# Kernel optimization log

Measured on AMD Instinct MI355X. Metric: run time of the kernel, lower is better.

Reference implementation:

```python
import jax, jax.numpy as jnp
import numpy as np

DIM = 1024
NUM_HEADS = 16
HEAD_DIM = DIM // NUM_HEADS  # 64
MAX_LABELS = 8
B, SQ, SKV = 2, 2048, 2048


def setup_inputs() -> dict:
    key = jax.random.key(0)
    ks = jax.random.split(key, 12)
    s = 0.02
    return {
        "visual_features": jax.random.normal(ks[0], (B, SQ, DIM), jnp.float32),
        "audio_features": jax.random.normal(ks[1], (B, SKV, DIM), jnp.float32),
        "audio_labels": jax.random.randint(ks[2], (B,), 0, MAX_LABELS),
        "Wq": jax.random.normal(ks[3], (DIM, DIM), jnp.float32) * s,
        "bq": jnp.zeros((DIM,), jnp.float32),
        "Wk": jax.random.normal(ks[4], (DIM, DIM), jnp.float32) * s,
        "bk": jnp.zeros((DIM,), jnp.float32),
        "Wv": jax.random.normal(ks[5], (DIM, DIM), jnp.float32) * s,
        "bv": jnp.zeros((DIM,), jnp.float32),
        "Wo": jax.random.normal(ks[6], (DIM, DIM), jnp.float32) * s,
        "bo": jnp.zeros((DIM,), jnp.float32),
        "label_emb": jax.random.normal(ks[7], (MAX_LABELS, HEAD_DIM), jnp.float32),
    }


def _lrope_emb(label_emb, labels, seq_len, dtype):
    # inv_freq over head_dim (buffer, recomputed)
    inv_freq = 1.0 / (10000.0 ** (jnp.arange(0, HEAD_DIM, 2, dtype=jnp.float32) / HEAD_DIM))
    pos = jnp.arange(seq_len, dtype=dtype)
    freqs = jnp.outer(pos, inv_freq)                       # [S, hd/2]
    emb = jnp.concatenate([jnp.sin(freqs), jnp.cos(freqs)], axis=-1)  # [S, hd]
    lab = label_emb[labels]                                # [B, hd]
    return emb[None, :, :] * lab[:, None, :]               # [B, S, hd]


def reference(visual_features, audio_features, audio_labels,
              Wq, bq, Wk, bk, Wv, bv, Wo, bo, label_emb):
    b, sq, _ = visual_features.shape
    skv = audio_features.shape[1]
    scale = HEAD_DIM ** -0.5

    q = visual_features @ Wq.T + bq                        # [B, Sq, D]
    k = audio_features @ Wk.T + bk                         # [B, Skv, D]
    v = audio_features @ Wv.T + bv

    q = q.reshape(b, sq, NUM_HEADS, HEAD_DIM)
    k = k.reshape(b, skv, NUM_HEADS, HEAD_DIM)
    v = v.reshape(b, skv, NUM_HEADS, HEAD_DIM)

    # L-RoPE additive embedding on K (per-head broadcast of the head_dim-sized emb)
    emb = _lrope_emb(label_emb, audio_labels, skv, k.dtype)  # [B, Skv, hd]
    k = k + emb[:, :, None, :]

    scores = jnp.einsum('bqhd,bkhd->bhqk', q, k) * scale   # [B, H, Sq, Skv]
    attn = jax.nn.softmax(scores, axis=-1)                 # dropout = identity (eval)
    out = jnp.einsum('bhqk,bkhd->bqhd', attn, v)           # [B, Sq, H, hd]
    out = out.reshape(b, sq, DIM)
    return out @ Wo.T + bo
```

## Files before the change

### kernel.cpp

```cpp
#include <hip/hip_runtime.h>
#include <hip/hip_bf16.h>


typedef short s16x8 __attribute__((ext_vector_type(8)));
typedef float f32x4 __attribute__((ext_vector_type(4)));

__device__ __forceinline__ short f2bf(float f) {
    unsigned u = __float_as_uint(f);
    u = u + 0x7fffu + ((u >> 16) & 1u);
    return (short)(u >> 16);
}

#define GLDS16(g, l)                                                          \
    __builtin_amdgcn_global_load_lds(                                         \
        (const __attribute__((address_space(1))) void*)(g),                   \
        (__attribute__((address_space(3))) void*)(l), 16, 0, 0)

__global__ __launch_bounds__(256)
void cvt_all(const float* __restrict__ vis, const float* __restrict__ aud,
             const float* __restrict__ Wq, const float* __restrict__ Wk,
             const float* __restrict__ Wv, const float* __restrict__ Wo,
             short* __restrict__ visB, short* __restrict__ audB,
             short* __restrict__ WqB, short* __restrict__ WkB,
             short* __restrict__ WvB, short* __restrict__ WoB)
{
    const int bid = blockIdx.x;
    const float* src; short* dst; int vec0;
    if (bid < 2048)      { src = vis; dst = visB; vec0 = bid * 256; }
    else if (bid < 4096) { src = aud; dst = audB; vec0 = (bid - 2048) * 256; }
    else {
        const int r = bid - 4096, w = r >> 9, lb = r & 511;
        vec0 = lb * 256;
        if      (w == 0) { src = Wq; dst = WqB; }
        else if (w == 1) { src = Wk; dst = WkB; }
        else if (w == 2) { src = Wv; dst = WvB; }
        else             { src = Wo; dst = WoB; }
    }
    const int i = (vec0 + threadIdx.x) * 8;
    float4 a = *(const float4*)(src + i);
    float4 b = *(const float4*)(src + i + 4);
    s16x8 o;
    o[0]=f2bf(a.x); o[1]=f2bf(a.y); o[2]=f2bf(a.z); o[3]=f2bf(a.w);
    o[4]=f2bf(b.x); o[5]=f2bf(b.y); o[6]=f2bf(b.z); o[7]=f2bf(b.w);
    *(s16x8*)(dst + i) = o;
}

__global__ __launch_bounds__(256)
void gemm_qkv(const short* __restrict__ visB, const short* __restrict__ audB,
              const short* __restrict__ WqB, const short* __restrict__ WkB,
              const short* __restrict__ WvB,
              const float* __restrict__ bq, const float* __restrict__ bk,
              const float* __restrict__ bv,
              short* __restrict__ outQ, short* __restrict__ outK,
              short* __restrict__ outVt,
              const int* __restrict__ labels, const float* __restrict__ lemb)
{
    __shared__ __align__(16) short As[2][128 * 64];
    __shared__ __align__(16) short Bs[2][128 * 64];
    const int tid  = threadIdx.x;
    const int lane = tid & 63;
    const int wid  = tid >> 6;
    const int z    = blockIdx.z;
    const int rowBase = blockIdx.y * 128;
    const int colBase = blockIdx.x * 128;
    const int wr = (wid >> 1) * 64;
    const int wc = (wid & 1) * 64;
    const short* X = (z == 0) ? visB : audB;
    const short* W = (z == 0) ? WqB : (z == 1) ? WkB : WvB;
    const float* bias = (z == 0) ? bq : (z == 1) ? bk : bv;

    f32x4 acc[4][4] = {};

    auto stage = [&](int buf, int k0) {
        #pragma unroll
        for (int c = 0; c < 4; ++c) {
            const int u   = (wid * 4 + c) * 64 + lane;
            const int row = u >> 3;
            const int k8a = (u & 7) ^ (row & 7);
            GLDS16(X + (size_t)(rowBase + row) * 1024 + k0 + k8a * 8,
                   &As[buf][(wid * 4 + c) * 512]);
            GLDS16(W + (size_t)(colBase + row) * 1024 + k0 + k8a * 8,
                   &Bs[buf][(wid * 4 + c) * 512]);
        }
    };

    stage(0, 0);
    __syncthreads();

    for (int t = 0; t < 16; ++t) {
        const int cur = t & 1;
        if (t < 15) stage(cur ^ 1, (t + 1) * 64);
        #pragma unroll
        for (int ks = 0; ks < 2; ++ks) {
            const int kb = ks * 64 + ((lane >> 4) << 4);
            s16x8 af[4], bfv[4];
            #pragma unroll
            for (int m = 0; m < 4; ++m) {
                const int row = wr + m * 16 + (lane & 15);
                af[m] = *(const s16x8*)((const char*)&As[cur][0] + row * 128 + (kb ^ ((row & 7) << 4)));
            }
            #pragma unroll
            for (int n = 0; n < 4; ++n) {
                const int row = wc + n * 16 + (lane & 15);
                bfv[n] = *(const s16x8*)((const char*)&Bs[cur][0] + row * 128 + (kb ^ ((row & 7) << 4)));
            }
            #pragma unroll
            for (int m = 0; m < 4; ++m)
                #pragma unroll
                for (int n = 0; n < 4; ++n)
                    acc[m][n] = __builtin_amdgcn_mfma_f32_16x16x32_bf16(af[m], bfv[n], acc[m][n], 0, 0, 0);
        }
        __syncthreads();
    }

    if (z == 2) {
        char* tb = (char*)&As[0][0] + wid * 8192;
        const int b  = rowBase >> 11;
        const int h  = (colBase + wc) >> 6;
        const int kvbase = (rowBase & 2047) + wr;
        #pragma unroll
        for (int m = 0; m < 4; ++m) {
            #pragma unroll
            for (int r = 0; r < 4; ++r) {
                const int kvl = m * 16 + ((lane >> 4) << 2) + r;
                #pragma unroll
                for (int n = 0; n < 4; ++n) {
                    const int hd = n * 16 + (lane & 15);
                    const float v = acc[m][n][r] + bias[colBase + wc + hd];
                    *(short*)(tb + hd * 128 + ((kvl * 2) ^ ((hd & 7) << 4))) = f2bf(v);
                }
            }
        }
        asm volatile("s_waitcnt lgkmcnt(0)" ::: "memory");
        #pragma unroll
        for (int c = 0; c < 8; ++c) {
            const int u  = c * 64 + lane;
            const int hd = u >> 3;
            const int kc = u & 7;
            s16x8 vv = *(const s16x8*)(tb + hd * 128 + ((kc * 16) ^ ((hd & 7) << 4)));
            *(s16x8*)(outVt + ((size_t)(b * 16 + h) * 64 + hd) * 2048 + kvbase + kc * 8) = vv;
        }
    } else {
        short* Co = (z == 0) ? outQ : outK;
        #pragma unroll
        for (int m = 0; m < 4; ++m) {
            #pragma unroll
            for (int r = 0; r < 4; ++r) {
                const int grow = rowBase + wr + m * 16 + ((lane >> 4) << 2) + r;
                #pragma unroll
                for (int n = 0; n < 4; ++n) {
                    const int gcol = colBase + wc + n * 16 + (lane & 15);
                    float v = acc[m][n][r] + bias[gcol];
                    if (z == 0) {
                        v *= 0.125f;
                    } else {
                        const int bb = grow >> 11;
                        const int ss = grow & 2047;
                        const int hd = gcol & 63;
                        const int fi = hd & 31;
                        const float ang = (float)ss * __expf((float)fi * (-9.210340371976184f / 32.0f));
                        const float tr  = (hd < 32) ? sinf(ang) : cosf(ang);
                        v += tr * lemb[labels[bb] * 64 + hd];
                    }
                    Co[(size_t)grow * 1024 + gcol] = f2bf(v);
                }
            }
        }
    }
}

__global__ __launch_bounds__(256)
void gemm_out(const short* __restrict__ X, const short* __restrict__ W,
              const float* __restrict__ bias, float* __restrict__ Cf)
{
    __shared__ __align__(16) short As[2][128 * 64];
    __shared__ __align__(16) short Bs[2][128 * 64];
    const int tid  = threadIdx.x;
    const int lane = tid & 63;
    const int wid  = tid >> 6;
    const int rowBase = blockIdx.y * 128;
    const int colBase = blockIdx.x * 128;
    const int wr = (wid >> 1) * 64;
    const int wc = (wid & 1) * 64;

    f32x4 acc[4][4] = {};

    auto stage = [&](int buf, int k0) {
        #pragma unroll
        for (int c = 0; c < 4; ++c) {
            const int u   = (wid * 4 + c) * 64 + lane;
            const int row = u >> 3;
            const int k8a = (u & 7) ^ (row & 7);
            GLDS16(X + (size_t)(rowBase + row) * 1024 + k0 + k8a * 8,
                   &As[buf][(wid * 4 + c) * 512]);
            GLDS16(W + (size_t)(colBase + row) * 1024 + k0 + k8a * 8,
                   &Bs[buf][(wid * 4 + c) * 512]);
        }
    };

    stage(0, 0);
    __syncthreads();

    for (int t = 0; t < 16; ++t) {
        const int cur = t & 1;
        if (t < 15) stage(cur ^ 1, (t + 1) * 64);
        #pragma unroll
        for (int ks = 0; ks < 2; ++ks) {
            const int kb = ks * 64 + ((lane >> 4) << 4);
            s16x8 af[4], bfv[4];
            #pragma unroll
            for (int m = 0; m < 4; ++m) {
                const int row = wr + m * 16 + (lane & 15);
                af[m] = *(const s16x8*)((const char*)&As[cur][0] + row * 128 + (kb ^ ((row & 7) << 4)));
            }
            #pragma unroll
            for (int n = 0; n < 4; ++n) {
                const int row = wc + n * 16 + (lane & 15);
                bfv[n] = *(const s16x8*)((const char*)&Bs[cur][0] + row * 128 + (kb ^ ((row & 7) << 4)));
            }
            #pragma unroll
            for (int m = 0; m < 4; ++m)
                #pragma unroll
                for (int n = 0; n < 4; ++n)
                    acc[m][n] = __builtin_amdgcn_mfma_f32_16x16x32_bf16(af[m], bfv[n], acc[m][n], 0, 0, 0);
        }
        __syncthreads();
    }

    #pragma unroll
    for (int m = 0; m < 4; ++m) {
        #pragma unroll
        for (int r = 0; r < 4; ++r) {
            const int grow = rowBase + wr + m * 16 + ((lane >> 4) << 2) + r;
            #pragma unroll
            for (int n = 0; n < 4; ++n) {
                const int gcol = colBase + wc + n * 16 + (lane & 15);
                Cf[(size_t)grow * 1024 + gcol] = acc[m][n][r] + bias[gcol];
            }
        }
    }
}

__global__ __launch_bounds__(256)
void attn_fwd(const short* __restrict__ Q, const short* __restrict__ K,
              const short* __restrict__ Vt, short* __restrict__ AO)
{
    __shared__ __align__(16) short Ks[2][64 * 64];
    __shared__ __align__(16) short Vs[2][64 * 64];
    __shared__ __align__(16) short Ps[4][16 * 64];
    const int tid  = threadIdx.x;
    const int lane = tid & 63;
    const int wid  = tid >> 6;
    const int qt = blockIdx.x;
    const int bh = blockIdx.y;
    const int b  = bh >> 4, h = bh & 15;
    const int qrow0 = b * 2048 + qt * 64;
    const int hoff  = h * 64;
    const short* Kb = K + (size_t)b * 2048 * 1024 + hoff;
    const short* Vb = Vt + (size_t)bh * 64 * 2048;

    s16x8 qf[2];
    {
        const int qr = qrow0 + wid * 16 + (lane & 15);
        const short* qp = Q + (size_t)qr * 1024 + hoff + ((lane >> 4) << 3);
        qf[0] = *(const s16x8*)(qp);
        qf[1] = *(const s16x8*)(qp + 32);
    }

    auto stage = [&](int buf, int kv0) {
        #pragma unroll
        for (int c = 0; c < 2; ++c) {
            const int ub  = c * 256 + wid * 64;
            const int u   = ub + lane;
            const int row = u >> 3;
            const int k8  = (u & 7) ^ (row & 7);
            GLDS16(Kb + (size_t)(kv0 + row) * 1024 + k8 * 8, &Ks[buf][ub * 8]);
            GLDS16(Vb + (size_t)row * 2048 + kv0 + k8 * 8,   &Vs[buf][ub * 8]);
        }
    };

    float mrun[4], lsum[4];
    f32x4 o[4] = {};
    #pragma unroll
    for (int r = 0; r < 4; ++r) { mrun[r] = -1e30f; lsum[r] = 0.f; }

    stage(0, 0);
    __syncthreads();

    for (int t = 0; t < 32; ++t) {
        const int cur = t & 1;
        if (t < 31) stage(cur ^ 1, (t + 1) * 64);

        f32x4 s[4] = {};
        #pragma unroll
        for (int ks = 0; ks < 2; ++ks) {
            const int kb = ks * 64 + ((lane >> 4) << 4);
            #pragma unroll
            for (int n = 0; n < 4; ++n) {
                const int row = n * 16 + (lane & 15);
                s16x8 kf = *(const s16x8*)((const char*)&Ks[cur][0] + row * 128 + (kb ^ ((row & 7) << 4)));
                s[n] = __builtin_amdgcn_mfma_f32_16x16x32_bf16(qf[ks], kf, s[n], 0, 0, 0);
            }
        }

        float pm[4];
        bool need = false;
        #pragma unroll
        for (int r = 0; r < 4; ++r) {
            pm[r] = fmaxf(fmaxf(s[0][r], s[1][r]), fmaxf(s[2][r], s[3][r]));
            need = need || (pm[r] > mrun[r] + 8.0f);
        }
        if (__any(need)) {
            #pragma unroll
            for (int r = 0; r < 4; ++r) {
                float t2 = pm[r];
                t2 = fmaxf(t2, __shfl_xor(t2, 1));
                t2 = fmaxf(t2, __shfl_xor(t2, 2));
                t2 = fmaxf(t2, __shfl_xor(t2, 4));
                t2 = fmaxf(t2, __shfl_xor(t2, 8));
                const float mn = fmaxf(mrun[r], t2);
                const float al = __expf(mrun[r] - mn);
                mrun[r] = mn;
                lsum[r] *= al;
                #pragma unroll
                for (int n = 0; n < 4; ++n) o[n][r] *= al;
            }
        }
        #pragma unroll
        for (int n = 0; n < 4; ++n) {
            #pragma unroll
            for (int r = 0; r < 4; ++r) {
                const float p = __expf(s[n][r] - mrun[r]);
                lsum[r] += p;
                const int row = ((lane >> 4) << 2) + r;
                const int col = n * 16 + (lane & 15);
                *(short*)((char*)&Ps[wid][0] + row * 128 + ((col * 2) ^ ((row & 7) << 4))) = f2bf(p);
            }
        }
        asm volatile("s_waitcnt lgkmcnt(0)" ::: "memory");

        #pragma unroll
        for (int ks = 0; ks < 2; ++ks) {
            const int kb = ks * 64 + ((lane >> 4) << 4);
            const int prow = lane & 15;
            s16x8 pa = *(const s16x8*)((const char*)&Ps[wid][0] + prow * 128 + (kb ^ ((prow & 7) << 4)));
            #pragma unroll
            for (int n = 0; n < 4; ++n) {
                const int row = n * 16 + (lane & 15);
                s16x8 vb = *(const s16x8*)((const char*)&Vs[cur][0] + row * 128 + (kb ^ ((row & 7) << 4)));
                o[n] = __builtin_amdgcn_mfma_f32_16x16x32_bf16(pa, vb, o[n], 0, 0, 0);
            }
        }
        __syncthreads();
    }

    #pragma unroll
    for (int r = 0; r < 4; ++r) {
        float tt = lsum[r];
        tt += __shfl_xor(tt, 1);
        tt += __shfl_xor(tt, 2);
        tt += __shfl_xor(tt, 4);
        tt += __shfl_xor(tt, 8);
        const float inv = 1.0f / tt;
        const int grow = qrow0 + wid * 16 + ((lane >> 4) << 2) + r;
        #pragma unroll
        for (int n = 0; n < 4; ++n) {
            const int gcol = hoff + n * 16 + (lane & 15);
            AO[(size_t)grow * 1024 + gcol] = f2bf(o[n][r] * inv);
        }
    }
}

extern "C" void kernel_launch(void* const* d_in, const int* in_sizes, int n_in,
                              void* d_out, int out_size, void* d_ws, size_t ws_size,
                              hipStream_t stream) {
    const float* vis    = (const float*)d_in[0];
    const float* aud    = (const float*)d_in[1];
    const int*   labels = (const int*)d_in[2];
    const float* Wq = (const float*)d_in[3];  const float* bq = (const float*)d_in[4];
    const float* Wk = (const float*)d_in[5];  const float* bk = (const float*)d_in[6];
    const float* Wv = (const float*)d_in[7];  const float* bv = (const float*)d_in[8];
    const float* Wo = (const float*)d_in[9];  const float* bo = (const float*)d_in[10];
    const float* lemb = (const float*)d_in[11];

    short* wsQ   = (short*)d_ws;
    short* wsK   = wsQ  + 4194304;
    short* wsVt  = wsK  + 4194304;
    short* wsAO  = wsVt + 4194304;
    short* visB  = wsAO + 4194304;
    short* audB  = visB + 4194304;
    short* WqB   = audB + 4194304;
    short* WkB   = WqB  + 1048576;
    short* WvB   = WkB  + 1048576;
    short* WoB   = WvB  + 1048576;
    float* out   = (float*)d_out;

    cvt_all<<<6144, 256, 0, stream>>>(vis, aud, Wq, Wk, Wv, Wo,
                                      visB, audB, WqB, WkB, WvB, WoB);
    gemm_qkv<<<dim3(8, 32, 3), 256, 0, stream>>>(visB, audB, WqB, WkB, WvB,
                                                 bq, bk, bv, wsQ, wsK, wsVt,
                                                 labels, lemb);
    attn_fwd<<<dim3(32, 32), 256, 0, stream>>>(wsQ, wsK, wsVt, wsAO);
    gemm_out<<<dim3(8, 32), 256, 0, stream>>>(wsAO, WoB, bo, out);
}
```

Measured before the change: 261.7 us.

## Halve GEMM row tiles and transpose S in attention for per-lane softmax

The QKV and output projection GEMMs move from 128x128 to 64x128 block tiles, doubling the grid for better occupancy and CU coverage at the cost of less operand reuse. The attention kernel computes S transposed (K as the A operand) so each lane owns one query row, which removes most cross-lane max and sum shuffles. It also packs P to bf16 with v_cvt_pk_bf16_f32 and writes it with 8-byte LDS stores instead of scalar shorts. Rescale factors are broadcast via shuffles, and the V transpose epilogue gains a barrier before reusing As.

```diff
diff --git a/kernel.cpp b/kernel.cpp
--- a/kernel.cpp
+++ b/kernel.cpp
@@ -9,6 +9,12 @@
     unsigned u = __float_as_uint(f);
     u = u + 0x7fffu + ((u >> 16) & 1u);
     return (short)(u >> 16);
+}
+
+__device__ __forceinline__ unsigned cvtpk(float lo, float hi) {
+    unsigned r;
+    asm volatile("v_cvt_pk_bf16_f32 %0, %1, %2" : "=v"(r) : "v"(lo), "v"(hi));
+    return r;
 }
 
 #define GLDS16(g, l)                                                          \
@@ -55,32 +61,40 @@
               short* __restrict__ outVt,
               const int* __restrict__ labels, const float* __restrict__ lemb)
 {
-    __shared__ __align__(16) short As[2][128 * 64];
+    __shared__ __align__(16) short As[2][64 * 64];
     __shared__ __align__(16) short Bs[2][128 * 64];
     const int tid  = threadIdx.x;
     const int lane = tid & 63;
     const int wid  = tid >> 6;
+    const int q15  = lane & 15;
+    const int hi   = lane >> 4;
     const int z    = blockIdx.z;
-    const int rowBase = blockIdx.y * 128;
+    const int rowBase = blockIdx.y * 64;
     const int colBase = blockIdx.x * 128;
-    const int wr = (wid >> 1) * 64;
+    const int wr = (wid >> 1) * 32;
     const int wc = (wid & 1) * 64;
     const short* X = (z == 0) ? visB : audB;
     const short* W = (z == 0) ? WqB : (z == 1) ? WkB : WvB;
     const float* bias = (z == 0) ? bq : (z == 1) ? bk : bv;
 
-    f32x4 acc[4][4] = {};
+    f32x4 acc[2][4] = {};
 
     auto stage = [&](int buf, int k0) {
         #pragma unroll
-        for (int c = 0; c < 4; ++c) {
-            const int u   = (wid * 4 + c) * 64 + lane;
+        for (int c = 0; c < 2; ++c) {
+            const int u   = c * 256 + tid;
             const int row = u >> 3;
             const int k8a = (u & 7) ^ (row & 7);
             GLDS16(X + (size_t)(rowBase + row) * 1024 + k0 + k8a * 8,
-                   &As[buf][(wid * 4 + c) * 512]);
+                   &As[buf][(c * 256 + wid * 64) * 8]);
+        }
+        #pragma unroll
+        for (int c = 0; c < 4; ++c) {
+            const int u   = c * 256 + tid;
+            const int row = u >> 3;
+            const int k8a = (u & 7) ^ (row & 7);
             GLDS16(W + (size_t)(colBase + row) * 1024 + k0 + k8a * 8,
-                   &Bs[buf][(wid * 4 + c) * 512]);
+                   &Bs[buf][(c * 256 + wid * 64) * 8]);
         }
     };
 
@@ -92,20 +106,20 @@
         if (t < 15) stage(cur ^ 1, (t + 1) * 64);
         #pragma unroll
         for (int ks = 0; ks < 2; ++ks) {
-            const int kb = ks * 64 + ((lane >> 4) << 4);
-            s16x8 af[4], bfv[4];
-            #pragma unroll
-            for (int m = 0; m < 4; ++m) {
-                const int row = wr + m * 16 + (lane & 15);
+            const int kb = ks * 64 + (hi << 4);
+            s16x8 af[2], bfv[4];
+            #pragma unroll
+            for (int m = 0; m < 2; ++m) {
+                const int row = wr + m * 16 + q15;
                 af[m] = *(const s16x8*)((const char*)&As[cur][0] + row * 128 + (kb ^ ((row & 7) << 4)));
             }
             #pragma unroll
             for (int n = 0; n < 4; ++n) {
-                const int row = wc + n * 16 + (lane & 15);
+                const int row = wc + n * 16 + q15;
                 bfv[n] = *(const s16x8*)((const char*)&Bs[cur][0] + row * 128 + (kb ^ ((row & 7) << 4)));
             }
             #pragma unroll
-            for (int m = 0; m < 4; ++m)
+            for (int m = 0; m < 2; ++m)
                 #pragma unroll
                 for (int n = 0; n < 4; ++n)
                     acc[m][n] = __builtin_amdgcn_mfma_f32_16x16x32_bf16(af[m], bfv[n], acc[m][n], 0, 0, 0);
@@ -114,42 +128,43 @@
     }
 
     if (z == 2) {
-        char* tb = (char*)&As[0][0] + wid * 8192;
+        __syncthreads();
+        char* tb = (char*)&As[0][0] + wid * 4096;
         const int b  = rowBase >> 11;
         const int h  = (colBase + wc) >> 6;
         const int kvbase = (rowBase & 2047) + wr;
         #pragma unroll
-        for (int m = 0; m < 4; ++m) {
+        for (int m = 0; m < 2; ++m) {
             #pragma unroll
             for (int r = 0; r < 4; ++r) {
-                const int kvl = m * 16 + ((lane >> 4) << 2) + r;
+                const int kvl = m * 16 + hi * 4 + r;
                 #pragma unroll
                 for (int n = 0; n < 4; ++n) {
-                    const int hd = n * 16 + (lane & 15);
+                    const int hd = n * 16 + q15;
                     const float v = acc[m][n][r] + bias[colBase + wc + hd];
-                    *(short*)(tb + hd * 128 + ((kvl * 2) ^ ((hd & 7) << 4))) = f2bf(v);
+                    *(short*)(tb + hd * 64 + ((kvl * 2) ^ ((hd & 3) << 4))) = f2bf(v);
                 }
             }
         }
         asm volatile("s_waitcnt lgkmcnt(0)" ::: "memory");
         #pragma unroll
-        for (int c = 0; c < 8; ++c) {
+        for (int c = 0; c < 4; ++c) {
             const int u  = c * 64 + lane;
-            const int hd = u >> 3;
-            const int kc = u & 7;
-            s16x8 vv = *(const s16x8*)(tb + hd * 128 + ((kc * 16) ^ ((hd & 7) << 4)));
+            const int hd = u >> 2;
+            const int kc = u & 3;
+            s16x8 vv = *(const s16x8*)(tb + hd * 64 + ((kc * 16) ^ ((hd & 3) << 4)));
             *(s16x8*)(outVt + ((size_t)(b * 16 + h) * 64 + hd) * 2048 + kvbase + kc * 8) = vv;
         }
     } else {
         short* Co = (z == 0) ? outQ : outK;
         #pragma unroll
-        for (int m = 0; m < 4; ++m) {
+        for (int m = 0; m < 2; ++m) {
             #pragma unroll
             for (int r = 0; r < 4; ++r) {
-                const int grow = rowBase + wr + m * 16 + ((lane >> 4) << 2) + r;
+                const int grow = rowBase + wr + m * 16 + hi * 4 + r;
                 #pragma unroll
                 for (int n = 0; n < 4; ++n) {
-                    const int gcol = colBase + wc + n * 16 + (lane & 15);
+                    const int gcol = colBase + wc + n * 16 + q15;
                     float v = acc[m][n][r] + bias[gcol];
                     if (z == 0) {
                         v *= 0.125f;
@@ -173,28 +188,36 @@
 void gemm_out(const short* __restrict__ X, const short* __restrict__ W,
               const float* __restrict__ bias, float* __restrict__ Cf)
 {
-    __shared__ __align__(16) short As[2][128 * 64];
+    __shared__ __align__(16) short As[2][64 * 64];
     __shared__ __align__(16) short Bs[2][128 * 64];
     const int tid  = threadIdx.x;
     const int lane = tid & 63;
     const int wid  = tid >> 6;
-    const int rowBase = blockIdx.y * 128;
+    const int q15  = lane & 15;
+    const int hi   = lane >> 4;
+    const int rowBase = blockIdx.y * 64;
     const int colBase = blockIdx.x * 128;
-    const int wr = (wid >> 1) * 64;
+    const int wr = (wid >> 1) * 32;
     const int wc = (wid & 1) * 64;
 
-    f32x4 acc[4][4] = {};
+    f32x4 acc[2][4] = {};
 
     auto stage = [&](int buf, int k0) {
         #pragma unroll
-        for (int c = 0; c < 4; ++c) {
-            const int u   = (wid * 4 + c) * 64 + lane;
+        for (int c = 0; c < 2; ++c) {
+            const int u   = c * 256 + tid;
             const int row = u >> 3;
             const int k8a = (u & 7) ^ (row & 7);
             GLDS16(X + (size_t)(rowBase + row) * 1024 + k0 + k8a * 8,
-                   &As[buf][(wid * 4 + c) * 512]);
+                   &As[buf][(c * 256 + wid * 64) * 8]);
+        }
+        #pragma unroll
+        for (int c = 0; c < 4; ++c) {
+            const int u   = c * 256 + tid;
+            const int row = u >> 3;
+            const int k8a = (u & 7) ^ (row & 7);
             GLDS16(W + (size_t)(colBase + row) * 1024 + k0 + k8a * 8,
-                   &Bs[buf][(wid * 4 + c) * 512]);
+                   &Bs[buf][(c * 256 + wid * 64) * 8]);
         }
     };
 
@@ -206,20 +229,20 @@
         if (t < 15) stage(cur ^ 1, (t + 1) * 64);
         #pragma unroll
         for (int ks = 0; ks < 2; ++ks) {
-            const int kb = ks * 64 + ((lane >> 4) << 4);
-            s16x8 af[4], bfv[4];
-            #pragma unroll
-            for (int m = 0; m < 4; ++m) {
-                const int row = wr + m * 16 + (lane & 15);
+            const int kb = ks * 64 + (hi << 4);
+            s16x8 af[2], bfv[4];
+            #pragma unroll
+            for (int m = 0; m < 2; ++m) {
+                const int row = wr + m * 16 + q15;
                 af[m] = *(const s16x8*)((const char*)&As[cur][0] + row * 128 + (kb ^ ((row & 7) << 4)));
             }
             #pragma unroll
             for (int n = 0; n < 4; ++n) {
-                const int row = wc + n * 16 + (lane & 15);
+                const int row = wc + n * 16 + q15;
                 bfv[n] = *(const s16x8*)((const char*)&Bs[cur][0] + row * 128 + (kb ^ ((row & 7) << 4)));
             }
             #pragma unroll
-            for (int m = 0; m < 4; ++m)
+            for (int m = 0; m < 2; ++m)
                 #pragma unroll
                 for (int n = 0; n < 4; ++n)
                     acc[m][n] = __builtin_amdgcn_mfma_f32_16x16x32_bf16(af[m], bfv[n], acc[m][n], 0, 0, 0);
@@ -228,13 +251,13 @@
     }
 
     #pragma unroll
-    for (int m = 0; m < 4; ++m) {
+    for (int m = 0; m < 2; ++m) {
         #pragma unroll
         for (int r = 0; r < 4; ++r) {
-            const int grow = rowBase + wr + m * 16 + ((lane >> 4) << 2) + r;
+            const int grow = rowBase + wr + m * 16 + hi * 4 + r;
             #pragma unroll
             for (int n = 0; n < 4; ++n) {
-                const int gcol = colBase + wc + n * 16 + (lane & 15);
+                const int gcol = colBase + wc + n * 16 + q15;
                 Cf[(size_t)grow * 1024 + gcol] = acc[m][n][r] + bias[gcol];
             }
         }
@@ -251,6 +274,8 @@
     const int tid  = threadIdx.x;
     const int lane = tid & 63;
     const int wid  = tid >> 6;
+    const int q15  = lane & 15;
+    const int hi   = lane >> 4;
     const int qt = blockIdx.x;
     const int bh = blockIdx.y;
     const int b  = bh >> 4, h = bh & 15;
@@ -258,11 +283,13 @@
     const int hoff  = h * 64;
     const short* Kb = K + (size_t)b * 2048 * 1024 + hoff;
     const short* Vb = Vt + (size_t)bh * 64 * 2048;
+    char* pw = (char*)&Ps[wid][0];
+    const int psw = (q15 & 7) << 4;
 
     s16x8 qf[2];
     {
-        const int qr = qrow0 + wid * 16 + (lane & 15);
-        const short* qp = Q + (size_t)qr * 1024 + hoff + ((lane >> 4) << 3);
+        const int qr = qrow0 + wid * 16 + q15;
+        const short* qp = Q + (size_t)qr * 1024 + hoff + hi * 8;
         qf[0] = *(const s16x8*)(qp);
         qf[1] = *(const s16x8*)(qp + 32);
     }
@@ -279,10 +306,8 @@
         }
     };
 
-    float mrun[4], lsum[4];
+    float mrun = -1e30f, lsum = 0.f;
     f32x4 o[4] = {};
-    #pragma unroll
-    for (int r = 0; r < 4; ++r) { mrun[r] = -1e30f; lsum[r] = 0.f; }
 
     stage(0, 0);
     __syncthreads();
@@ -294,59 +319,56 @@
         f32x4 s[4] = {};
         #pragma unroll
         for (int ks = 0; ks < 2; ++ks) {
-            const int kb = ks * 64 + ((lane >> 4) << 4);
+            const int kb = ks * 64 + (hi << 4);
             #pragma unroll
             for (int n = 0; n < 4; ++n) {
-                const int row = n * 16 + (lane & 15);
+                const int row = n * 16 + q15;
                 s16x8 kf = *(const s16x8*)((const char*)&Ks[cur][0] + row * 128 + (kb ^ ((row & 7) << 4)));
-                s[n] = __builtin_amdgcn_mfma_f32_16x16x32_bf16(qf[ks], kf, s[n], 0, 0, 0);
-            }
-        }
-
-        float pm[4];
-        bool need = false;
-        #pragma unroll
-        for (int r = 0; r < 4; ++r) {
-            pm[r] = fmaxf(fmaxf(s[0][r], s[1][r]), fmaxf(s[2][r], s[3][r]));
-            need = need || (pm[r] > mrun[r] + 8.0f);
-        }
-        if (__any(need)) {
-            #pragma unroll
-            for (int r = 0; r < 4; ++r) {
-                float t2 = pm[r];
-                t2 = fmaxf(t2, __shfl_xor(t2, 1));
-                t2 = fmaxf(t2, __shfl_xor(t2, 2));
-                t2 = fmaxf(t2, __shfl_xor(t2, 4));
-                t2 = fmaxf(t2, __shfl_xor(t2, 8));
-                const float mn = fmaxf(mrun[r], t2);
-                const float al = __expf(mrun[r] - mn);
-                mrun[r] = mn;
-                lsum[r] *= al;
+                s[n] = __builtin_amdgcn_mfma_f32_16x16x32_bf16(kf, qf[ks], s[n], 0, 0, 0);
+            }
+        }
+
+        float pm = s[0][0];
+        #pragma unroll
+        for (int n = 0; n < 4; ++n)
+            #pragma unroll
+            for (int r = 0; r < 4; ++r) pm = fmaxf(pm, s[n][r]);
+        if (__any(pm > mrun + 8.0f)) {
+            float t2 = fmaxf(pm, __shfl_xor(pm, 16));
+            t2 = fmaxf(t2, __shfl_xor(t2, 32));
+            const float mn = fmaxf(mrun, t2);
+            const float al = __expf(mrun - mn);
+            mrun = mn;
+            lsum *= al;
+            float alq[4];
+            #pragma unroll
+            for (int r = 0; r < 4; ++r) alq[r] = __shfl(al, hi * 4 + r);
+            #pragma unroll
+            for (int n = 0; n < 4; ++n)
                 #pragma unroll
-                for (int n = 0; n < 4; ++n) o[n][r] *= al;
-            }
+                for (int r = 0; r < 4; ++r) o[n][r] *= alq[r];
         }
         #pragma unroll
         for (int n = 0; n < 4; ++n) {
-            #pragma unroll
-            for (int r = 0; r < 4; ++r) {
-                const float p = __expf(s[n][r] - mrun[r]);
-                lsum[r] += p;
-                const int row = ((lane >> 4) << 2) + r;
-                const int col = n * 16 + (lane & 15);
-                *(short*)((char*)&Ps[wid][0] + row * 128 + ((col * 2) ^ ((row & 7) << 4))) = f2bf(p);
-            }
+            float p0 = __expf(s[n][0] - mrun);
+            float p1 = __expf(s[n][1] - mrun);
+            float p2 = __expf(s[n][2] - mrun);
+            float p3 = __expf(s[n][3] - mrun);
+            lsum += (p0 + p1) + (p2 + p3);
+            uint2 pk;
+            pk.x = cvtpk(p0, p1);
+            pk.y = cvtpk(p2, p3);
+            *(uint2*)(pw + q15 * 128 + ((n * 32 + hi * 8) ^ psw)) = pk;
         }
         asm volatile("s_waitcnt lgkmcnt(0)" ::: "memory");
 
         #pragma unroll
         for (int ks = 0; ks < 2; ++ks) {
-            const int kb = ks * 64 + ((lane >> 4) << 4);
-            const int prow = lane & 15;
-            s16x8 pa = *(const s16x8*)((const char*)&Ps[wid][0] + prow * 128 + (kb ^ ((prow & 7) << 4)));
+            const int kb = ks * 64 + (hi << 4);
+            s16x8 pa = *(const s16x8*)(pw + q15 * 128 + ((ks * 64 + hi * 16) ^ psw));
             #pragma unroll
             for (int n = 0; n < 4; ++n) {
-                const int row = n * 16 + (lane & 15);
+                const int row = n * 16 + q15;
                 s16x8 vb = *(const s16x8*)((const char*)&Vs[cur][0] + row * 128 + (kb ^ ((row & 7) << 4)));
                 o[n] = __builtin_amdgcn_mfma_f32_16x16x32_bf16(pa, vb, o[n], 0, 0, 0);
             }
@@ -354,19 +376,20 @@
         __syncthreads();
     }
 
+    float tt = lsum;
+    tt += __shfl_xor(tt, 16);
+    tt += __shfl_xor(tt, 32);
+    const float inv = 1.0f / tt;
+    float invq[4];
+    #pragma unroll
+    for (int r = 0; r < 4; ++r) invq[r] = __shfl(inv, hi * 4 + r);
     #pragma unroll
     for (int r = 0; r < 4; ++r) {
-        float tt = lsum[r];
-        tt += __shfl_xor(tt, 1);
-        tt += __shfl_xor(tt, 2);
-        tt += __shfl_xor(tt, 4);
-        tt += __shfl_xor(tt, 8);
-        const float inv = 1.0f / tt;
-        const int grow = qrow0 + wid * 16 + ((lane >> 4) << 2) + r;
+        const int grow = qrow0 + wid * 16 + hi * 4 + r;
         #pragma unroll
         for (int n = 0; n < 4; ++n) {
-            const int gcol = hoff + n * 16 + (lane & 15);
-            AO[(size_t)grow * 1024 + gcol] = f2bf(o[n][r] * inv);
+            const int gcol = hoff + n * 16 + q15;
+            AO[(size_t)grow * 1024 + gcol] = f2bf(o[n][r] * invq[r]);
         }
     }
 }
@@ -397,9 +420,9 @@
 
     cvt_all<<<6144, 256, 0, stream>>>(vis, aud, Wq, Wk, Wv, Wo,
                                       visB, audB, WqB, WkB, WvB, WoB);
-    gemm_qkv<<<dim3(8, 32, 3), 256, 0, stream>>>(visB, audB, WqB, WkB, WvB,
+    gemm_qkv<<<dim3(8, 64, 3), 256, 0, stream>>>(visB, audB, WqB, WkB, WvB,
                                                  bq, bk, bv, wsQ, wsK, wsVt,
                                                  labels, lemb);
     attn_fwd<<<dim3(32, 32), 256, 0, stream>>>(wsQ, wsK, wsVt, wsAO);
-    gemm_out<<<dim3(8, 32), 256, 0, stream>>>(wsAO, WoB, bo, out);
-}
+    gemm_out<<<dim3(8, 64), 256, 0, stream>>>(wsAO, WoB, bo, out);
+}
```

New measurement: 248.9 us. 1.05x faster.
